# Kernel tuning notes

Hardware: AMD Instinct MI355X
Metric: run time of the kernel (lower is better)

The kernel has to match this reference:

```python
import jax, jax.numpy as jnp
import numpy as np

EMBED_DIM = 768
NUM_HEADS = 12
HEAD_DIM = EMBED_DIM // NUM_HEADS


def setup_inputs() -> dict:
    key = jax.random.key(0)
    ks = jax.random.split(key, 9)
    d = EMBED_DIM
    s = 1.0 / np.sqrt(d)
    x = jax.random.normal(ks[0], (1, 4096, d), dtype=jnp.float32)
    # nn.Linear weights stored as [out, in]; init ~ U(-1/sqrt(in), 1/sqrt(in))
    wq = jax.random.uniform(ks[1], (d, d), jnp.float32, -s, s)
    bq = jax.random.uniform(ks[2], (d,), jnp.float32, -s, s)
    wk = jax.random.uniform(ks[3], (d, d), jnp.float32, -s, s)
    bk = jax.random.uniform(ks[4], (d,), jnp.float32, -s, s)
    wv = jax.random.uniform(ks[5], (d, d), jnp.float32, -s, s)
    bv = jax.random.uniform(ks[6], (d,), jnp.float32, -s, s)
    ww = jax.random.uniform(ks[7], (d, d), jnp.float32, -s, s)
    bw = jax.random.uniform(ks[8], (d,), jnp.float32, -s, s)
    return {"x": x, "wq": wq, "bq": bq, "wk": wk, "bk": bk,
            "wv": wv, "bv": bv, "ww": ww, "bw": bw}


def reference(x, wq, bq, wk, bk, wv, bv, ww, bw):
    B, S, D = x.shape
    H, Hd = NUM_HEADS, HEAD_DIM
    # Linear: x @ W^T + b, then split heads -> [B, H, S, Hd]
    def proj(w, b):
        y = x @ w.T + b
        return y.reshape(B, S, H, Hd).transpose(0, 2, 1, 3)
    q = proj(wq, bq)
    k = proj(wk, bk)
    v = proj(wv, bv)
    scores = jnp.einsum('bhqd,bhkd->bhqk', q, k) / jnp.sqrt(jnp.float32(Hd))
    attn = jax.nn.softmax(scores, axis=-1)
    out = jnp.einsum('bhqk,bhkd->bhqd', attn, v)  # [B,H,S,Hd]
    out = out.transpose(0, 2, 1, 3).reshape(B, S, D)
    return out @ ww.T + bw
```

## Files before the change

### kernel.cpp

```cpp
#include <hip/hip_runtime.h>
#include <cstdio>


using u16 = unsigned short;
typedef __bf16 bf16x8 __attribute__((ext_vector_type(8)));
typedef float f32x4 __attribute__((ext_vector_type(4)));
typedef float f32x16 __attribute__((ext_vector_type(16)));
typedef unsigned int u32x4 __attribute__((ext_vector_type(4)));
typedef u16 u16x4 __attribute__((ext_vector_type(4)));

constexpr int SEQ = 4096;
constexpr int DIM = 768;
constexpr int NH = 12;
constexpr int HD = 64;
constexpr int LDT = 72;
constexpr int LDA2 = 40;
constexpr int LDM = 68;
constexpr float SM_PRE = 0.18033688011112042f;

__device__ __forceinline__ u16 f2bf(float f) {
  union { float f; unsigned u; } v{f};
  unsigned r = v.u + 0x7fffu + ((v.u >> 16) & 1u);
  return (u16)(r >> 16);
}
__device__ __forceinline__ unsigned cvtpk_bf16(float a, float b) {
  unsigned r;
  asm("v_cvt_pk_bf16_f32 %0, %1, %2" : "=v"(r) : "v"(a), "v"(b));
  return r;
}
__device__ __forceinline__ void swap32(unsigned& a, unsigned& b) {
  asm volatile("v_permlane32_swap_b32 %0, %1" : "+v"(a), "+v"(b));
}
__device__ __forceinline__ bf16x8 bc16(const u16* p) {
  return __builtin_bit_cast(bf16x8, *(const u32x4*)p);
}
__device__ __forceinline__ float partner32(float v, int hi) {
  unsigned a = __builtin_bit_cast(unsigned, v), b = a;
  swap32(a, b);
  return __builtin_bit_cast(float, hi ? a : b);
}

__global__ __launch_bounds__(256) void qkv_gemm(const float* __restrict__ x,
                                                const float* __restrict__ wq,
                                                const float* __restrict__ wk,
                                                const float* __restrict__ wv,
                                                const float* __restrict__ bq,
                                                const float* __restrict__ bk,
                                                const float* __restrict__ bv,
                                                u16* __restrict__ Qb,
                                                u16* __restrict__ Kb,
                                                u16* __restrict__ Vtb) {
  __shared__ alignas(16) u16 As[2][64 * LDA2];
  __shared__ alignas(16) u16 Bq[2][64 * LDA2];
  __shared__ alignas(16) u16 Bk[2][64 * LDA2];
  __shared__ alignas(16) u16 Bv[2][64 * LDA2];

  const int tid = threadIdx.x, lane = tid & 63, wave = tid >> 6;
  const int lg = lane >> 4, ln = lane & 15;
  const int bid = blockIdx.x;
  const int swz = (bid & 7) * 96 + (bid >> 3);
  const int mt = swz / 12, nt = swz % 12;
  const int m0 = mt * 64, n0 = nt * 64;
  const int srow = tid >> 2, scol = (tid & 3) * 8;

  f32x4 acc[4][3] = {};

  float4 a0, a1, q0, q1, k0, k1, v0, v1;
  auto pf = [&](int kk) {
    const float* ap = x + (size_t)(m0 + srow) * DIM + kk + scol;
    a0 = *(const float4*)ap; a1 = *(const float4*)(ap + 4);
    const size_t wb = (size_t)(n0 + srow) * DIM + kk + scol;
    q0 = *(const float4*)(wq + wb); q1 = *(const float4*)(wq + wb + 4);
    k0 = *(const float4*)(wk + wb); k1 = *(const float4*)(wk + wb + 4);
    v0 = *(const float4*)(wv + wb); v1 = *(const float4*)(wv + wb + 4);
  };
  auto stage = [&](int b) {
    *(u32x4*)&As[b][srow * LDA2 + scol] =
        u32x4{cvtpk_bf16(a0.x, a0.y), cvtpk_bf16(a0.z, a0.w),
              cvtpk_bf16(a1.x, a1.y), cvtpk_bf16(a1.z, a1.w)};
    *(u32x4*)&Bq[b][srow * LDA2 + scol] =
        u32x4{cvtpk_bf16(q0.x, q0.y), cvtpk_bf16(q0.z, q0.w),
              cvtpk_bf16(q1.x, q1.y), cvtpk_bf16(q1.z, q1.w)};
    *(u32x4*)&Bk[b][srow * LDA2 + scol] =
        u32x4{cvtpk_bf16(k0.x, k0.y), cvtpk_bf16(k0.z, k0.w),
              cvtpk_bf16(k1.x, k1.y), cvtpk_bf16(k1.z, k1.w)};
    *(u32x4*)&Bv[b][srow * LDA2 + scol] =
        u32x4{cvtpk_bf16(v0.x, v0.y), cvtpk_bf16(v0.z, v0.w),
              cvtpk_bf16(v1.x, v1.y), cvtpk_bf16(v1.z, v1.w)};
  };

  constexpr int NS = DIM / 32;
  pf(0);
  stage(0);
  pf(32);
  __syncthreads();

  for (int s = 0; s < NS; ++s) {
    const int cur = s & 1;
    bf16x8 a[4];
#pragma unroll
    for (int i = 0; i < 4; ++i)
      a[i] = bc16(&As[cur][(i * 16 + ln) * LDA2 + lg * 8]);
    bf16x8 fq = bc16(&Bq[cur][(wave * 16 + ln) * LDA2 + lg * 8]);
    bf16x8 fk = bc16(&Bk[cur][(wave * 16 + ln) * LDA2 + lg * 8]);
    bf16x8 fv = bc16(&Bv[cur][(wave * 16 + ln) * LDA2 + lg * 8]);
    if (s + 1 < NS) {
      stage(cur ^ 1);
      if (s + 2 < NS) pf((s + 2) * 32);
    }
#pragma unroll
    for (int i = 0; i < 4; ++i) {
      acc[i][0] = __builtin_amdgcn_mfma_f32_16x16x32_bf16(a[i], fq, acc[i][0], 0, 0, 0);
      acc[i][1] = __builtin_amdgcn_mfma_f32_16x16x32_bf16(a[i], fk, acc[i][1], 0, 0, 0);
      acc[i][2] = __builtin_amdgcn_mfma_f32_16x16x32_bf16(a[i], fv, acc[i][2], 0, 0, 0);
    }
    __syncthreads();
  }

  const int col = n0 + wave * 16 + ln;
  const float bvq = bq[col], bvk = bk[col], bvv = bv[col];
#pragma unroll
  for (int i = 0; i < 4; ++i) {
    const int rowb = m0 + i * 16 + lg * 4;
#pragma unroll
    for (int r = 0; r < 4; ++r) {
      Qb[(size_t)(rowb + r) * DIM + col] = f2bf((acc[i][0][r] + bvq) * SM_PRE);
      Kb[(size_t)(rowb + r) * DIM + col] = f2bf(acc[i][1][r] + bvk);
    }
    u16x4 pk;
#pragma unroll
    for (int r = 0; r < 4; ++r) pk[r] = f2bf(acc[i][2][r] + bvv);
    *(u16x4*)&Vtb[(size_t)col * SEQ + rowb] = pk;
  }
}

__global__ __launch_bounds__(256) void out_gemm(const u16* __restrict__ Ab,
                                                const float* __restrict__ W,
                                                const float* __restrict__ bias,
                                                float* __restrict__ out) {
  __shared__ alignas(16) u16 As[2][64 * LDA2];
  __shared__ alignas(16) u16 Bs[2][64 * LDA2];

  const int tid = threadIdx.x, lane = tid & 63, wave = tid >> 6;
  const int lg = lane >> 4, ln = lane & 15;
  const int bid = blockIdx.x;
  const int swz = (bid & 7) * 96 + (bid >> 3);
  const int mt = swz / 12, nt = swz % 12;
  const int m0 = mt * 64, n0 = nt * 64;
  const int srow = tid >> 2, scol = (tid & 3) * 8;

  f32x4 acc[4] = {};

  u32x4 pA;
  float4 pB0, pB1;
  auto pf = [&](int kk) {
    pA = *(const u32x4*)(Ab + (size_t)(m0 + srow) * DIM + kk + scol);
    const float* w = W + (size_t)(n0 + srow) * DIM + kk + scol;
    pB0 = *(const float4*)w;
    pB1 = *(const float4*)(w + 4);
  };
  auto stage = [&](int b) {
    *(u32x4*)&As[b][srow * LDA2 + scol] = pA;
    *(u32x4*)&Bs[b][srow * LDA2 + scol] =
        u32x4{cvtpk_bf16(pB0.x, pB0.y), cvtpk_bf16(pB0.z, pB0.w),
              cvtpk_bf16(pB1.x, pB1.y), cvtpk_bf16(pB1.z, pB1.w)};
  };

  constexpr int NS = DIM / 32;
  pf(0);
  stage(0);
  pf(32);
  __syncthreads();

  for (int s = 0; s < NS; ++s) {
    const int cur = s & 1;
    bf16x8 b = bc16(&Bs[cur][(wave * 16 + ln) * LDA2 + lg * 8]);
    bf16x8 a[4];
#pragma unroll
    for (int j = 0; j < 4; ++j)
      a[j] = bc16(&As[cur][(j * 16 + ln) * LDA2 + lg * 8]);
    if (s + 1 < NS) {
      stage(cur ^ 1);
      if (s + 2 < NS) pf((s + 2) * 32);
    }
#pragma unroll
    for (int j = 0; j < 4; ++j)
      acc[j] = __builtin_amdgcn_mfma_f32_16x16x32_bf16(a[j], b, acc[j], 0, 0, 0);
    __syncthreads();
  }

  const int col = n0 + wave * 16 + ln;
  const float bv = bias[col];
#pragma unroll
  for (int j = 0; j < 4; ++j) {
    const int rowb = m0 + j * 16 + lg * 4;
#pragma unroll
    for (int r = 0; r < 4; ++r) out[(size_t)(rowb + r) * DIM + col] = acc[j][r] + bv;
  }
}

__global__ __launch_bounds__(256, 3) void attn_kernel(const u16* __restrict__ Q,
                                                      const u16* __restrict__ K,
                                                      const u16* __restrict__ Vt,
                                                      u16* __restrict__ AO) {
  __shared__ alignas(16) u16 Ks[2][64 * LDT];
  __shared__ alignas(16) u16 Vs[2][64 * LDT];
  __shared__ float slx[4][32];

  const int tid = threadIdx.x, lane = tid & 63, wave = tid >> 6;
  const int l31 = lane & 31, hi = lane >> 5;
  const int g = wave >> 1, p = wave & 1;
  const int bid = blockIdx.x;
  const int swz = (bid & 7) * 96 + (bid >> 3);
  const int h = swz >> 6;
  const int q0 = (swz & 63) * 64;
  const int qw = q0 + g * 32;

  bf16x8 qf[4];
#pragma unroll
  for (int c = 0; c < 4; ++c)
    qf[c] = bc16(Q + (size_t)(qw + l31) * DIM + h * HD + c * 16 + hi * 8);

  float l_ = 0.f;
  f32x16 oacc[2] = {};

  const int srow = tid >> 2;
  const int scol = (tid & 3) * 16;
  const u16* Kh = K + (size_t)h * HD;
  const u16* Vh = Vt + (size_t)h * HD * SEQ;
  constexpr int NT = SEQ / 64;

  u32x4 kp0, kp1, vp0, vp1;
  auto pf = [&](int t) {
    const u32x4* s = (const u32x4*)(Kh + (size_t)(t * 64 + srow) * DIM + scol);
    kp0 = s[0]; kp1 = s[1];
    const u32x4* v = (const u32x4*)(Vh + (size_t)srow * SEQ + t * 64 + scol);
    vp0 = v[0]; vp1 = v[1];
  };
  auto stage = [&](int buf) {
    u16* kd = &Ks[buf][srow * LDT + scol];
    *(u32x4*)kd = kp0; *(u32x4*)(kd + 8) = kp1;
    u16* vd = &Vs[buf][srow * LDT + scol];
    *(u32x4*)vd = vp0; *(u32x4*)(vd + 8) = vp1;
  };

  pf(0);
  stage(0);
  pf(1);
  __syncthreads();

  auto round = [&](int t, int cur) {
    const int kr = (p * 32 + l31) * LDT + hi * 8;
    bf16x8 kf0 = bc16(&Ks[cur][kr]);
    bf16x8 kf1 = bc16(&Ks[cur][kr + 16]);
    bf16x8 kf2 = bc16(&Ks[cur][kr + 32]);
    bf16x8 kf3 = bc16(&Ks[cur][kr + 48]);
    const int vr0 = l31 * LDT + p * 32 + hi * 8;
    const int vr1 = (32 + l31) * LDT + p * 32 + hi * 8;
    bf16x8 vf00 = bc16(&Vs[cur][vr0]);
    bf16x8 vf01 = bc16(&Vs[cur][vr0 + 16]);
    bf16x8 vf10 = bc16(&Vs[cur][vr1]);
    bf16x8 vf11 = bc16(&Vs[cur][vr1 + 16]);

    if (t + 1 < NT) {
      stage(cur ^ 1);
      pf(t + 2 < NT ? t + 2 : t + 1);
    }

    f32x16 st = {};
    __builtin_amdgcn_s_setprio(1);
    st = __builtin_amdgcn_mfma_f32_32x32x16_bf16(kf0, qf[0], st, 0, 0, 0);
    st = __builtin_amdgcn_mfma_f32_32x32x16_bf16(kf1, qf[1], st, 0, 0, 0);
    st = __builtin_amdgcn_mfma_f32_32x32x16_bf16(kf2, qf[2], st, 0, 0, 0);
    st = __builtin_amdgcn_mfma_f32_32x32x16_bf16(kf3, qf[3], st, 0, 0, 0);
    __builtin_amdgcn_s_setprio(0);

#pragma unroll
    for (int r = 0; r < 16; ++r) st[r] = __builtin_amdgcn_exp2f(st[r]);

    {
      float s0 = (st[0] + st[4]) + (st[8] + st[12]);
      float s1 = (st[1] + st[5]) + (st[9] + st[13]);
      float s2 = (st[2] + st[6]) + (st[10] + st[14]);
      float s3 = (st[3] + st[7]) + (st[11] + st[15]);
      float rs = (s0 + s1) + (s2 + s3);
      l_ += rs + partner32(rs, hi);
    }

    unsigned c0 = cvtpk_bf16(st[0], st[1]), c1 = cvtpk_bf16(st[2], st[3]);
    unsigned c2 = cvtpk_bf16(st[4], st[5]), c3 = cvtpk_bf16(st[6], st[7]);
    unsigned c4 = cvtpk_bf16(st[8], st[9]), c5 = cvtpk_bf16(st[10], st[11]);
    unsigned c6 = cvtpk_bf16(st[12], st[13]), c7 = cvtpk_bf16(st[14], st[15]);
    swap32(c0, c2); swap32(c1, c3); swap32(c4, c6); swap32(c5, c7);
    bf16x8 pa0 = __builtin_bit_cast(bf16x8, u32x4{c0, c1, c2, c3});
    bf16x8 pa1 = __builtin_bit_cast(bf16x8, u32x4{c4, c5, c6, c7});

    __builtin_amdgcn_s_setprio(1);
    oacc[0] = __builtin_amdgcn_mfma_f32_32x32x16_bf16(pa0, vf00, oacc[0], 0, 0, 0);
    oacc[0] = __builtin_amdgcn_mfma_f32_32x32x16_bf16(pa1, vf01, oacc[0], 0, 0, 0);
    oacc[1] = __builtin_amdgcn_mfma_f32_32x32x16_bf16(pa0, vf10, oacc[1], 0, 0, 0);
    oacc[1] = __builtin_amdgcn_mfma_f32_32x32x16_bf16(pa1, vf11, oacc[1], 0, 0, 0);
    __builtin_amdgcn_s_setprio(0);
    __syncthreads();
  };

  for (int t = 0; t < NT; t += 2) {
    round(t, 0);
    round(t + 1, 1);
  }

  if (hi == 0) slx[wave][l31] = l_;
  __syncthreads();

  const float L = slx[g * 2][l31] + slx[g * 2 + 1][l31];
  const float Linv = 1.f / L;
  float Lr[16];
#pragma unroll
  for (int r = 0; r < 16; ++r)
    Lr[r] = __shfl(Linv, (r & 3) + 8 * (r >> 2) + 4 * hi);

  float* Om = (float*)Ks;
  if (p == 1) {
#pragma unroll
    for (int nd = 0; nd < 2; ++nd)
#pragma unroll
      for (int r = 0; r < 16; ++r) {
        const int row = (r & 3) + 8 * (r >> 2) + 4 * hi;
        Om[(g * 32 + row) * LDM + nd * 32 + l31] = oacc[nd][r];
      }
  }
  __syncthreads();
  if (p == 0) {
#pragma unroll
    for (int nd = 0; nd < 2; ++nd)
#pragma unroll
      for (int r = 0; r < 16; ++r) {
        const int row = (r & 3) + 8 * (r >> 2) + 4 * hi;
        const float v =
            (oacc[nd][r] + Om[(g * 32 + row) * LDM + nd * 32 + l31]) * Lr[r];
        AO[(size_t)(qw + row) * DIM + h * HD + nd * 32 + l31] = f2bf(v);
      }
  }
}

extern "C" void kernel_launch(void* const* d_in, const int* in_sizes, int n_in,
                              void* d_out, int out_size, void* d_ws, size_t ws_size,
                              hipStream_t stream) {
  const float* x = (const float*)d_in[0];
  const float* wq = (const float*)d_in[1];
  const float* bq = (const float*)d_in[2];
  const float* wk = (const float*)d_in[3];
  const float* bk = (const float*)d_in[4];
  const float* wv = (const float*)d_in[5];
  const float* bv = (const float*)d_in[6];
  const float* ww = (const float*)d_in[7];
  const float* bw = (const float*)d_in[8];

  const size_t mat = (size_t)SEQ * DIM;
  if (ws_size < 4 * mat * sizeof(u16)) {
    fprintf(stderr, "kernel_launch: ws too small (%zu)\n", ws_size);
    return;
  }
  u16* Qb = (u16*)d_ws;
  u16* Kb = Qb + mat;
  u16* Vtb = Kb + mat;
  u16* AOb = Vtb + mat;

  qkv_gemm<<<dim3(768), dim3(256), 0, stream>>>(x, wq, wk, wv, bq, bk, bv, Qb, Kb, Vtb);
  attn_kernel<<<dim3(768), dim3(256), 0, stream>>>(Qb, Kb, Vtb, AOb);
  out_gemm<<<dim3(768), dim3(256), 0, stream>>>(AOb, ww, bw, (float*)d_out);
}
```

Measured before the change: 125.4 us.

## Pre-convert inputs and weights to bf16 MFMA fragment layout in prep kernels

Adds prep kernels that convert x to bf16 and rearrange the Q/K/V/out weights into a bf16 per-wave MFMA fragment layout. The GEMMs then load B fragments straight from global memory into registers, double-buffered, with no LDS staging and no conversion in the inner loop. This cuts LDS traffic and the repeated fp32->bf16 conversion of weights across blocks. The cost is two extra launches and extra global round trips. Scratch space is reused from the output buffer and from the K and AO workspaces, which relies on careful ordering.

```diff
diff --git a/kernel.cpp b/kernel.cpp
--- a/kernel.cpp
+++ b/kernel.cpp
@@ -16,6 +16,7 @@
 constexpr int LDT = 72;
 constexpr int LDA2 = 40;
 constexpr int LDM = 68;
+constexpr int NKS = DIM / 32;
 constexpr float SM_PRE = 0.18033688011112042f;
 
 __device__ __forceinline__ u16 f2bf(float f) {
@@ -40,10 +41,54 @@
   return __builtin_bit_cast(float, hi ? a : b);
 }
 
-__global__ __launch_bounds__(256) void qkv_gemm(const float* __restrict__ x,
+__device__ __forceinline__ void wfrag_store(const float* __restrict__ w,
+                                            u16* __restrict__ wf, int widx) {
+  const int lane = widx & 63;
+  const int ks = (widx >> 6) % NKS;
+  const int nt = widx / (64 * NKS);
+  const int n_abs = nt * 16 + (lane & 15);
+  const int k0 = ks * 32 + (lane >> 4) * 8;
+  const float* s = w + (size_t)n_abs * DIM + k0;
+  float4 f0 = *(const float4*)s, f1 = *(const float4*)(s + 4);
+  *(u32x4*)(wf + (size_t)widx * 8) =
+      u32x4{cvtpk_bf16(f0.x, f0.y), cvtpk_bf16(f0.z, f0.w),
+            cvtpk_bf16(f1.x, f1.y), cvtpk_bf16(f1.z, f1.w)};
+}
+
+__global__ __launch_bounds__(256) void prep_all(const float* __restrict__ x,
                                                 const float* __restrict__ wq,
                                                 const float* __restrict__ wk,
                                                 const float* __restrict__ wv,
+                                                u16* __restrict__ xb,
+                                                u16* __restrict__ wqf,
+                                                u16* __restrict__ wkf,
+                                                u16* __restrict__ wvf) {
+  const int blk = blockIdx.x;
+  if (blk < 1536) {
+    size_t i = ((size_t)blk * 256 + threadIdx.x) * 8;
+    float4 f0 = *(const float4*)(x + i);
+    float4 f1 = *(const float4*)(x + i + 4);
+    *(u32x4*)(xb + i) = u32x4{cvtpk_bf16(f0.x, f0.y), cvtpk_bf16(f0.z, f0.w),
+                              cvtpk_bf16(f1.x, f1.y), cvtpk_bf16(f1.z, f1.w)};
+  } else {
+    const int wi = blk - 1536;
+    const int mat = wi / 288;
+    const int widx = (wi % 288) * 256 + threadIdx.x;
+    const float* src = mat == 0 ? wq : (mat == 1 ? wk : wv);
+    u16* dst = mat == 0 ? wqf : (mat == 1 ? wkf : wvf);
+    wfrag_store(src, dst, widx);
+  }
+}
+
+__global__ __launch_bounds__(256) void prep_wfrag(const float* __restrict__ w,
+                                                  u16* __restrict__ wf) {
+  wfrag_store(w, wf, blockIdx.x * 256 + threadIdx.x);
+}
+
+__global__ __launch_bounds__(256) void qkv_gemm(const u16* __restrict__ xb,
+                                                const u16* __restrict__ wqf,
+                                                const u16* __restrict__ wkf,
+                                                const u16* __restrict__ wvf,
                                                 const float* __restrict__ bq,
                                                 const float* __restrict__ bk,
                                                 const float* __restrict__ bv,
@@ -51,9 +96,6 @@
                                                 u16* __restrict__ Kb,
                                                 u16* __restrict__ Vtb) {
   __shared__ alignas(16) u16 As[2][64 * LDA2];
-  __shared__ alignas(16) u16 Bq[2][64 * LDA2];
-  __shared__ alignas(16) u16 Bk[2][64 * LDA2];
-  __shared__ alignas(16) u16 Bv[2][64 * LDA2];
 
   const int tid = threadIdx.x, lane = tid & 63, wave = tid >> 6;
   const int lg = lane >> 4, ln = lane & 15;
@@ -65,56 +107,54 @@
 
   f32x4 acc[4][3] = {};
 
-  float4 a0, a1, q0, q1, k0, k1, v0, v1;
-  auto pf = [&](int kk) {
-    const float* ap = x + (size_t)(m0 + srow) * DIM + kk + scol;
-    a0 = *(const float4*)ap; a1 = *(const float4*)(ap + 4);
-    const size_t wb = (size_t)(n0 + srow) * DIM + kk + scol;
-    q0 = *(const float4*)(wq + wb); q1 = *(const float4*)(wq + wb + 4);
-    k0 = *(const float4*)(wk + wb); k1 = *(const float4*)(wk + wb + 4);
-    v0 = *(const float4*)(wv + wb); v1 = *(const float4*)(wv + wb + 4);
-  };
-  auto stage = [&](int b) {
-    *(u32x4*)&As[b][srow * LDA2 + scol] =
-        u32x4{cvtpk_bf16(a0.x, a0.y), cvtpk_bf16(a0.z, a0.w),
-              cvtpk_bf16(a1.x, a1.y), cvtpk_bf16(a1.z, a1.w)};
-    *(u32x4*)&Bq[b][srow * LDA2 + scol] =
-        u32x4{cvtpk_bf16(q0.x, q0.y), cvtpk_bf16(q0.z, q0.w),
-              cvtpk_bf16(q1.x, q1.y), cvtpk_bf16(q1.z, q1.w)};
-    *(u32x4*)&Bk[b][srow * LDA2 + scol] =
-        u32x4{cvtpk_bf16(k0.x, k0.y), cvtpk_bf16(k0.z, k0.w),
-              cvtpk_bf16(k1.x, k1.y), cvtpk_bf16(k1.z, k1.w)};
-    *(u32x4*)&Bv[b][srow * LDA2 + scol] =
-        u32x4{cvtpk_bf16(v0.x, v0.y), cvtpk_bf16(v0.z, v0.w),
-              cvtpk_bf16(v1.x, v1.y), cvtpk_bf16(v1.z, v1.w)};
-  };
-
-  constexpr int NS = DIM / 32;
-  pf(0);
-  stage(0);
-  pf(32);
-  __syncthreads();
-
-  for (int s = 0; s < NS; ++s) {
-    const int cur = s & 1;
+  u32x4 pA;
+  auto pfA = [&](int kk) {
+    pA = *(const u32x4*)(xb + (size_t)(m0 + srow) * DIM + kk + scol);
+  };
+  auto stageA = [&](int b) { *(u32x4*)&As[b][srow * LDA2 + scol] = pA; };
+
+  const size_t fb = (size_t)(n0 / 16 + wave) * NKS * 512 + (size_t)lane * 8;
+  auto ldB = [&](int s, u32x4& q, u32x4& k, u32x4& v) {
+    const size_t off = fb + (size_t)s * 512;
+    q = *(const u32x4*)(wqf + off);
+    k = *(const u32x4*)(wkf + off);
+    v = *(const u32x4*)(wvf + off);
+  };
+
+  auto body = [&](int s, int cur, u32x4& fQ, u32x4& fK, u32x4& fV) {
     bf16x8 a[4];
 #pragma unroll
     for (int i = 0; i < 4; ++i)
       a[i] = bc16(&As[cur][(i * 16 + ln) * LDA2 + lg * 8]);
-    bf16x8 fq = bc16(&Bq[cur][(wave * 16 + ln) * LDA2 + lg * 8]);
-    bf16x8 fk = bc16(&Bk[cur][(wave * 16 + ln) * LDA2 + lg * 8]);
-    bf16x8 fv = bc16(&Bv[cur][(wave * 16 + ln) * LDA2 + lg * 8]);
-    if (s + 1 < NS) {
-      stage(cur ^ 1);
-      if (s + 2 < NS) pf((s + 2) * 32);
-    }
+    if (s + 1 < NKS) {
+      stageA(cur ^ 1);
+      if (s + 2 < NKS) pfA((s + 2) * 32);
+    }
+    bf16x8 bq_ = __builtin_bit_cast(bf16x8, fQ);
+    bf16x8 bk_ = __builtin_bit_cast(bf16x8, fK);
+    bf16x8 bv_ = __builtin_bit_cast(bf16x8, fV);
 #pragma unroll
     for (int i = 0; i < 4; ++i) {
-      acc[i][0] = __builtin_amdgcn_mfma_f32_16x16x32_bf16(a[i], fq, acc[i][0], 0, 0, 0);
-      acc[i][1] = __builtin_amdgcn_mfma_f32_16x16x32_bf16(a[i], fk, acc[i][1], 0, 0, 0);
-      acc[i][2] = __builtin_amdgcn_mfma_f32_16x16x32_bf16(a[i], fv, acc[i][2], 0, 0, 0);
+      acc[i][0] = __builtin_amdgcn_mfma_f32_16x16x32_bf16(a[i], bq_, acc[i][0], 0, 0, 0);
+      acc[i][1] = __builtin_amdgcn_mfma_f32_16x16x32_bf16(a[i], bk_, acc[i][1], 0, 0, 0);
+      acc[i][2] = __builtin_amdgcn_mfma_f32_16x16x32_bf16(a[i], bv_, acc[i][2], 0, 0, 0);
     }
     __syncthreads();
+  };
+
+  pfA(0);
+  stageA(0);
+  pfA(32);
+  u32x4 q0, k0, v0, q1, k1, v1;
+  ldB(0, q0, k0, v0);
+  ldB(1, q1, k1, v1);
+  __syncthreads();
+
+  for (int s = 0; s < NKS; s += 2) {
+    body(s, 0, q0, k0, v0);
+    if (s + 2 < NKS) ldB(s + 2, q0, k0, v0);
+    body(s + 1, 1, q1, k1, v1);
+    if (s + 3 < NKS) ldB(s + 3, q1, k1, v1);
   }
 
   const int col = n0 + wave * 16 + ln;
@@ -135,11 +175,10 @@
 }
 
 __global__ __launch_bounds__(256) void out_gemm(const u16* __restrict__ Ab,
-                                                const float* __restrict__ W,
+                                                const u16* __restrict__ wf,
                                                 const float* __restrict__ bias,
                                                 float* __restrict__ out) {
   __shared__ alignas(16) u16 As[2][64 * LDA2];
-  __shared__ alignas(16) u16 Bs[2][64 * LDA2];
 
   const int tid = threadIdx.x, lane = tid & 63, wave = tid >> 6;
   const int lg = lane >> 4, ln = lane & 15;
@@ -152,41 +191,43 @@
   f32x4 acc[4] = {};
 
   u32x4 pA;
-  float4 pB0, pB1;
-  auto pf = [&](int kk) {
+  auto pfA = [&](int kk) {
     pA = *(const u32x4*)(Ab + (size_t)(m0 + srow) * DIM + kk + scol);
-    const float* w = W + (size_t)(n0 + srow) * DIM + kk + scol;
-    pB0 = *(const float4*)w;
-    pB1 = *(const float4*)(w + 4);
-  };
-  auto stage = [&](int b) {
-    *(u32x4*)&As[b][srow * LDA2 + scol] = pA;
-    *(u32x4*)&Bs[b][srow * LDA2 + scol] =
-        u32x4{cvtpk_bf16(pB0.x, pB0.y), cvtpk_bf16(pB0.z, pB0.w),
-              cvtpk_bf16(pB1.x, pB1.y), cvtpk_bf16(pB1.z, pB1.w)};
-  };
-
-  constexpr int NS = DIM / 32;
-  pf(0);
-  stage(0);
-  pf(32);
-  __syncthreads();
-
-  for (int s = 0; s < NS; ++s) {
-    const int cur = s & 1;
-    bf16x8 b = bc16(&Bs[cur][(wave * 16 + ln) * LDA2 + lg * 8]);
+  };
+  auto stageA = [&](int b) { *(u32x4*)&As[b][srow * LDA2 + scol] = pA; };
+
+  const size_t fb = (size_t)(n0 / 16 + wave) * NKS * 512 + (size_t)lane * 8;
+  auto ldW = [&](int s, u32x4& q) { q = *(const u32x4*)(wf + fb + (size_t)s * 512); };
+
+  auto body = [&](int s, int cur, u32x4& fW) {
     bf16x8 a[4];
 #pragma unroll
     for (int j = 0; j < 4; ++j)
       a[j] = bc16(&As[cur][(j * 16 + ln) * LDA2 + lg * 8]);
-    if (s + 1 < NS) {
-      stage(cur ^ 1);
-      if (s + 2 < NS) pf((s + 2) * 32);
-    }
+    if (s + 1 < NKS) {
+      stageA(cur ^ 1);
+      if (s + 2 < NKS) pfA((s + 2) * 32);
+    }
+    bf16x8 b = __builtin_bit_cast(bf16x8, fW);
 #pragma unroll
     for (int j = 0; j < 4; ++j)
       acc[j] = __builtin_amdgcn_mfma_f32_16x16x32_bf16(a[j], b, acc[j], 0, 0, 0);
     __syncthreads();
+  };
+
+  pfA(0);
+  stageA(0);
+  pfA(32);
+  u32x4 w0, w1;
+  ldW(0, w0);
+  ldW(1, w1);
+  __syncthreads();
+
+  for (int s = 0; s < NKS; s += 2) {
+    body(s, 0, w0);
+    if (s + 2 < NKS) ldW(s + 2, w0);
+    body(s + 1, 1, w1);
+    if (s + 3 < NKS) ldW(s + 3, w1);
   }
 
   const int col = n0 + wave * 16 + ln;
@@ -357,6 +398,7 @@
   const float* bw = (const float*)d_in[8];
 
   const size_t mat = (size_t)SEQ * DIM;
+  const size_t nw = (size_t)DIM * DIM;
   if (ws_size < 4 * mat * sizeof(u16)) {
     fprintf(stderr, "kernel_launch: ws too small (%zu)\n", ws_size);
     return;
@@ -365,8 +407,15 @@
   u16* Kb = Qb + mat;
   u16* Vtb = Kb + mat;
   u16* AOb = Vtb + mat;
-
-  qkv_gemm<<<dim3(768), dim3(256), 0, stream>>>(x, wq, wk, wv, bq, bk, bv, Qb, Kb, Vtb);
+  u16* xb = AOb;
+  u16* wqf = (u16*)d_out;
+  u16* wkf = wqf + nw;
+  u16* wvf = wkf + nw;
+  u16* wwf = Kb;
+
+  prep_all<<<dim3(2400), dim3(256), 0, stream>>>(x, wq, wk, wv, xb, wqf, wkf, wvf);
+  qkv_gemm<<<dim3(768), dim3(256), 0, stream>>>(xb, wqf, wkf, wvf, bq, bk, bv, Qb, Kb, Vtb);
   attn_kernel<<<dim3(768), dim3(256), 0, stream>>>(Qb, Kb, Vtb, AOb);
-  out_gemm<<<dim3(768), dim3(256), 0, stream>>>(AOb, ww, bw, (float*)d_out);
-}
+  prep_wfrag<<<dim3(288), dim3(256), 0, stream>>>(ww, wwf);
+  out_gemm<<<dim3(768), dim3(256), 0, stream>>>(AOb, wwf, bw, (float*)d_out);
+}
```

Result: faster. 115.2 us (-8.1%).
